# Optimization experiments

Measured on AMD Instinct MI355X. Metric: run time of the kernel, lower is better.

The kernel has to match this reference:

```python
import jax, jax.numpy as jnp
import numpy as np

N, K, D = 65536, 1024, 512


def setup_inputs() -> dict:
    key = jax.random.key(0)
    kx, kc, kv, kp = jax.random.split(key, 4)
    X = jax.random.normal(kx, (N, D), dtype=jnp.float32)
    center = jax.random.normal(kc, (K, D), dtype=jnp.float32)
    var = jax.random.uniform(kv, (K,), dtype=jnp.float32)
    pr = jax.random.uniform(kp, (K,), dtype=jnp.float32)
    threshold = jnp.zeros((1,), dtype=jnp.float32)
    return {"X": X, "center": center, "var": var, "pr": pr, "threshold": threshold}


def reference(X, center, var, pr, threshold):
    # Pairwise squared distances [N, K] via the expanded form
    # avoids materializing the N x K x D tensor).
    x_sq = jnp.sum(X * X, axis=-1, keepdims=True)            # [N, 1]
    c_sq = jnp.sum(center * center, axis=-1)                  # [K]
    cross = jnp.einsum('nd,kd->nk', X, center)                # [N, K]
    sqdist = x_sq - 2.0 * cross + c_sq[None, :]               # [N, K]
    # density: reciprocal-distance weighted sum with weights pr * var
    density = jnp.reciprocal(sqdist) @ (pr * var)             # [N]
    return density - threshold                                 # [N] (threshold [1] broadcasts)
```

## Files before the change

kernel.cpp:

```cpp
#include <hip/hip_runtime.h>
#include <stdint.h>


#define NR 65536
#define KC 1024
#define DD 512

#define BM 256
#define BN 256
#define BK 64
#define NKT (DD / BK)
#define NPART (KC / BN)

#define SLOT_SZ 65536
#define PART_OFF 131072
#define LDS_TOTAL (PART_OFF + 4096)

typedef __bf16 bf16;
typedef __attribute__((ext_vector_type(4))) __bf16 bf16x4;
typedef __attribute__((ext_vector_type(8))) __bf16 bf16x8;
typedef __attribute__((ext_vector_type(4))) float f32x4;

__device__ __forceinline__ void gload16(const void* g, void* l) {
  __builtin_amdgcn_global_load_lds(
      (const __attribute__((address_space(1))) unsigned int*)g,
      (__attribute__((address_space(3))) unsigned int*)l, 16, 0, 0);
}

__global__ __launch_bounds__(256) void prep_kernel(
    const float* __restrict__ X, const float* __restrict__ C,
    const float* __restrict__ var, const float* __restrict__ pr,
    bf16* __restrict__ Xb, bf16* __restrict__ Cb,
    float* __restrict__ xsq, float* __restrict__ csq, float* __restrict__ w) {
  const int row  = (int)((blockIdx.x * 256 + threadIdx.x) >> 6);
  const int lane = (int)(threadIdx.x & 63);
  const bool isX = row < NR;
  const float* srow = isX ? (X + (size_t)row * DD) : (C + (size_t)(row - NR) * DD);
  bf16* drow = isX ? (Xb + (size_t)row * DD) : (Cb + (size_t)(row - NR) * DD);

  float4 a = reinterpret_cast<const float4*>(srow)[lane];
  float4 b = reinterpret_cast<const float4*>(srow)[64 + lane];
  float s = a.x * a.x + a.y * a.y + a.z * a.z + a.w * a.w +
            b.x * b.x + b.y * b.y + b.z * b.z + b.w * b.w;
#pragma unroll
  for (int off = 1; off < 64; off <<= 1) s += __shfl_xor(s, off, 64);

  bf16x4 va = {(bf16)a.x, (bf16)a.y, (bf16)a.z, (bf16)a.w};
  bf16x4 vb = {(bf16)b.x, (bf16)b.y, (bf16)b.z, (bf16)b.w};
  reinterpret_cast<bf16x4*>(drow)[lane]      = va;
  reinterpret_cast<bf16x4*>(drow)[64 + lane] = vb;

  if (lane == 0) {
    if (isX) {
      xsq[row] = s;
    } else {
      const int k = row - NR;
      csq[k] = s;
      w[k]   = pr[k] * var[k];
    }
  }
}


#define STAGE_A(h, tn, slotW)                                                   \
  gload16(aSrc0 + (size_t)((h) * 64) * DD + (tn) * 64,                          \
          smem + (slotW) + (h) * 16384 + wid * 1024);                           \
  gload16(aSrc0 + (size_t)((h) * 64 + 128) * DD + (tn) * 64,                    \
          smem + (slotW) + (h) * 16384 + 8192 + wid * 1024);

#define STAGE_B(kk, tn, slotW)                                                  \
  gload16(bSrc0 + (tn) * 64 + (kk) * 32,                                        \
          smem + (slotW) + 32768 + (kk) * 16384 + wid * 1024);                  \
  gload16(bSrc0 + (size_t)128 * DD + (tn) * 64 + (kk) * 32,                     \
          smem + (slotW) + 32768 + (kk) * 16384 + 8192 + wid * 1024);

#define READ_B(dst, kk, base)                                                   \
  _Pragma("unroll") for (int n = 0; n < 4; ++n)                                 \
    dst[n] = *(const bf16x8*)(smem + (base) + 32768 + (kk) * 16384 + bRd +      \
                              n * 1024);

__global__ __launch_bounds__(512, 2) void density_kernel(
    const bf16* __restrict__ Xb, const bf16* __restrict__ Cb,
    const float* __restrict__ xsq, const float* __restrict__ csq,
    const float* __restrict__ w, float* __restrict__ partial) {
  extern __shared__ char smem[];

  const int tid  = (int)threadIdx.x;
  const int lane = tid & 63;
  const int wid  = tid >> 6;
  const int wr   = wid >> 2;
  const int wcn  = wid & 3;
  const int lr   = lane & 15;
  const int lc   = lane >> 4;

  const int bid   = (int)blockIdx.x;
  const int swz   = (bid & 7) * 128 + (bid >> 3);
  const int ntile = swz >> 8;
  const int mtile = swz & 255;
  const int rowBase = mtile * BM;
  const int colBase = ntile * BN;

  const bf16* aSrc0 = Xb + (size_t)(rowBase + wid * 8 + (lane >> 3)) * DD +
                      (((lane & 7) ^ (lane >> 3)) << 3);
  const bf16* bSrc0 = Cb + (size_t)(colBase + wid * 16 + (lane >> 2)) * DD +
                      ((((lane & 3) ^ ((lane >> 3) & 3))) << 3);

  const int aRd  = (wr * 64 + lr) * 128;
  const int aSw0 = ((lc ^ (lr & 7)) << 4);
  const int aSw1 = (((4 | lc) ^ (lr & 7)) << 4);
  const int bRd  = (wcn * 64 + lr) * 64 + ((lc ^ ((lr >> 1) & 3)) << 4);

  f32x4 acc[8][4];
#pragma unroll
  for (int m = 0; m < 8; ++m)
#pragma unroll
    for (int n = 0; n < 4; ++n) acc[m][n] = (f32x4){0.f, 0.f, 0.f, 0.f};

  bf16x8 bgK0[4], bgK1[4];

  STAGE_A(0, 0, 0);
  STAGE_B(0, 0, 0);
  STAGE_A(1, 0, 0);
  STAGE_B(1, 0, 0);
  asm volatile("s_waitcnt vmcnt(0)");
  __builtin_amdgcn_s_barrier();

#pragma unroll 1
  for (int t = 0; t < NKT; ++t) {
    const int slotR = (t & 1) << 16;
    const int slotW = slotR ^ SLOT_SZ;
    const int tn = t + 1;
    const bool st = tn < NKT;

    if (st) {
      STAGE_A(0, tn, slotW);
      STAGE_B(0, tn, slotW);
      STAGE_A(1, tn, slotW);
      STAGE_B(1, tn, slotW);
    }

    READ_B(bgK0, 0, slotR);
    READ_B(bgK1, 1, slotR);

    __builtin_amdgcn_s_setprio(1);
#pragma unroll
    for (int h = 0; h < 2; ++h) {
#pragma unroll
      for (int mi = 0; mi < 4; ++mi) {
        const bf16x8 a0 = *(const bf16x8*)(smem + slotR + h * 16384 + aRd +
                                           mi * 2048 + aSw0);
        const bf16x8 a1 = *(const bf16x8*)(smem + slotR + h * 16384 + aRd +
                                           mi * 2048 + aSw1);
#pragma unroll
        for (int n = 0; n < 4; ++n)
          acc[h * 4 + mi][n] = __builtin_amdgcn_mfma_f32_16x16x32_bf16(
              a0, bgK0[n], acc[h * 4 + mi][n], 0, 0, 0);
#pragma unroll
        for (int n = 0; n < 4; ++n)
          acc[h * 4 + mi][n] = __builtin_amdgcn_mfma_f32_16x16x32_bf16(
              a1, bgK1[n], acc[h * 4 + mi][n], 0, 0, 0);
      }
    }
    __builtin_amdgcn_s_setprio(0);

    if (st) {
      asm volatile("s_waitcnt vmcnt(0)");
      __builtin_amdgcn_s_barrier();
    }
  }

  float xr[8][4];
#pragma unroll
  for (int m = 0; m < 8; ++m)
#pragma unroll
    for (int j = 0; j < 4; ++j)
      xr[m][j] = xsq[rowBase + wr * 128 + m * 16 + lc * 4 + j];

  float rsum[8][4];
#pragma unroll
  for (int m = 0; m < 8; ++m)
#pragma unroll
    for (int j = 0; j < 4; ++j) rsum[m][j] = 0.f;

#pragma unroll
  for (int n = 0; n < 4; ++n) {
    const int gc = colBase + wcn * 64 + n * 16 + lr;
    const float cs = csq[gc];
    const float ww = w[gc];
#pragma unroll
    for (int m = 0; m < 8; ++m)
#pragma unroll
      for (int j = 0; j < 4; ++j) {
        const float sq = xr[m][j] + cs - 2.f * acc[m][n][j];
        rsum[m][j] += ww * __builtin_amdgcn_rcpf(sq);
      }
  }
#pragma unroll
  for (int m = 0; m < 8; ++m)
#pragma unroll
    for (int j = 0; j < 4; ++j) {
      float v = rsum[m][j];
      v += __shfl_xor(v, 1, 64);
      v += __shfl_xor(v, 2, 64);
      v += __shfl_xor(v, 4, 64);
      v += __shfl_xor(v, 8, 64);
      rsum[m][j] = v;
    }

  float* part = (float*)(smem + PART_OFF);
  __syncthreads();
  if (lr == 0) {
#pragma unroll
    for (int m = 0; m < 8; ++m)
#pragma unroll
      for (int j = 0; j < 4; ++j)
        part[wcn * 256 + wr * 128 + m * 16 + lc * 4 + j] = rsum[m][j];
  }
  __syncthreads();
  if (tid < BM) {
    const float s = part[tid] + part[256 + tid] + part[512 + tid] + part[768 + tid];
    partial[(size_t)ntile * NR + rowBase + tid] = s;
  }
}

__global__ __launch_bounds__(256) void reduce_kernel(
    const float* __restrict__ partial, const float* __restrict__ thr,
    float* __restrict__ out) {
  const int n = (int)(blockIdx.x * 256 + threadIdx.x);
  float s = 0.f;
#pragma unroll
  for (int g = 0; g < NPART; ++g) s += partial[(size_t)g * NR + n];
  out[n] = s - thr[0];
}

extern "C" void kernel_launch(void* const* d_in, const int* in_sizes, int n_in,
                              void* d_out, int out_size, void* d_ws, size_t ws_size,
                              hipStream_t stream) {
  const float* X   = (const float*)d_in[0];
  const float* C   = (const float*)d_in[1];
  const float* var = (const float*)d_in[2];
  const float* pr  = (const float*)d_in[3];
  const float* thr = (const float*)d_in[4];
  float* out = (float*)d_out;

  char* ws = (char*)d_ws;
  bf16* Xb   = (bf16*)(ws);
  bf16* Cb   = (bf16*)(ws + (size_t)NR * DD * 2);
  float* xsq = (float*)(ws + (size_t)NR * DD * 2 + (size_t)KC * DD * 2);
  float* csq = xsq + NR;
  float* w   = csq + KC;
  float* partial = w + KC;

  prep_kernel<<<(NR + KC) / 4, 256, 0, stream>>>(X, C, var, pr, Xb, Cb, xsq, csq, w);
  density_kernel<<<(NR / BM) * NPART, 512, LDS_TOTAL, stream>>>(
      Xb, Cb, xsq, csq, w, partial);
  reduce_kernel<<<NR / 256, 256, 0, stream>>>(partial, thr, out);
}
```

Before: 114.8 us.

## Shrink density GEMM tile to 128x256 with BK=32 and four waves

Reworks the density GEMM tiling from 256x256 blocks of 8 waves with BK=64 to 128x256 blocks of 4 waves with BK=32. LDS use drops from about 132KB to about 50KB, and the grid doubles to 2048 blocks, so more blocks can be resident per CU and waves are spread more evenly across CUs. The cost is lower arithmetic intensity per block, more X/C reloads from L2, and twice as many k-iterations, each with its own barrier.

```diff
diff --git a/kernel.cpp b/kernel.cpp
--- a/kernel.cpp
+++ b/kernel.cpp
@@ -6,15 +6,15 @@
 #define KC 1024
 #define DD 512
 
-#define BM 256
+#define BM 128
 #define BN 256
-#define BK 64
+#define BK 32
 #define NKT (DD / BK)
 #define NPART (KC / BN)
 
-#define SLOT_SZ 65536
-#define PART_OFF 131072
-#define LDS_TOTAL (PART_OFF + 4096)
+#define SLOT_SZ 24576
+#define PART_OFF 49152
+#define LDS_TOTAL (PART_OFF + 2048)
 
 typedef __bf16 bf16;
 typedef __attribute__((ext_vector_type(4))) __bf16 bf16x4;
@@ -62,24 +62,19 @@
 }
 
 
-#define STAGE_A(h, tn, slotW)                                                   \
-  gload16(aSrc0 + (size_t)((h) * 64) * DD + (tn) * 64,                          \
-          smem + (slotW) + (h) * 16384 + wid * 1024);                           \
-  gload16(aSrc0 + (size_t)((h) * 64 + 128) * DD + (tn) * 64,                    \
-          smem + (slotW) + (h) * 16384 + 8192 + wid * 1024);
-
-#define STAGE_B(kk, tn, slotW)                                                  \
-  gload16(bSrc0 + (tn) * 64 + (kk) * 32,                                        \
-          smem + (slotW) + 32768 + (kk) * 16384 + wid * 1024);                  \
-  gload16(bSrc0 + (size_t)128 * DD + (tn) * 64 + (kk) * 32,                     \
-          smem + (slotW) + 32768 + (kk) * 16384 + 8192 + wid * 1024);
-
-#define READ_B(dst, kk, base)                                                   \
-  _Pragma("unroll") for (int n = 0; n < 4; ++n)                                 \
-    dst[n] = *(const bf16x8*)(smem + (base) + 32768 + (kk) * 16384 + bRd +      \
-                              n * 1024);
-
-__global__ __launch_bounds__(512, 2) void density_kernel(
+#define STAGE(tn, slotW)                                                        \
+  gload16(aSrc0 + (tn) * 32,                smem + (slotW) + wid * 1024);       \
+  gload16(aSrc0 + (size_t)64 * DD + (tn) * 32,                                  \
+          smem + (slotW) + 4096 + wid * 1024);                                  \
+  gload16(bSrc0 + (tn) * 32,                smem + (slotW) + 8192 + wid * 1024);\
+  gload16(bSrc0 + (size_t)64 * DD + (tn) * 32,                                  \
+          smem + (slotW) + 12288 + wid * 1024);                                 \
+  gload16(bSrc0 + (size_t)128 * DD + (tn) * 32,                                 \
+          smem + (slotW) + 16384 + wid * 1024);                                 \
+  gload16(bSrc0 + (size_t)192 * DD + (tn) * 32,                                 \
+          smem + (slotW) + 20480 + wid * 1024);
+
+__global__ __launch_bounds__(256, 2) void density_kernel(
     const bf16* __restrict__ Xb, const bf16* __restrict__ Cb,
     const float* __restrict__ xsq, const float* __restrict__ csq,
     const float* __restrict__ w, float* __restrict__ partial) {
@@ -88,27 +83,23 @@
   const int tid  = (int)threadIdx.x;
   const int lane = tid & 63;
   const int wid  = tid >> 6;
-  const int wr   = wid >> 2;
-  const int wcn  = wid & 3;
   const int lr   = lane & 15;
   const int lc   = lane >> 4;
 
   const int bid   = (int)blockIdx.x;
-  const int swz   = (bid & 7) * 128 + (bid >> 3);
-  const int ntile = swz >> 8;
-  const int mtile = swz & 255;
+  const int swz   = (bid & 7) * 256 + (bid >> 3);
+  const int ntile = swz >> 9;
+  const int mtile = swz & 511;
   const int rowBase = mtile * BM;
   const int colBase = ntile * BN;
 
-  const bf16* aSrc0 = Xb + (size_t)(rowBase + wid * 8 + (lane >> 3)) * DD +
-                      (((lane & 7) ^ (lane >> 3)) << 3);
-  const bf16* bSrc0 = Cb + (size_t)(colBase + wid * 16 + (lane >> 2)) * DD +
-                      ((((lane & 3) ^ ((lane >> 3) & 3))) << 3);
-
-  const int aRd  = (wr * 64 + lr) * 128;
-  const int aSw0 = ((lc ^ (lr & 7)) << 4);
-  const int aSw1 = (((4 | lc) ^ (lr & 7)) << 4);
-  const int bRd  = (wcn * 64 + lr) * 64 + ((lc ^ ((lr >> 1) & 3)) << 4);
+  const int chunkSw = (((lane & 3) ^ ((lane >> 3) & 3)) << 3);
+  const bf16* aSrc0 = Xb + (size_t)(rowBase + wid * 16 + (lane >> 2)) * DD + chunkSw;
+  const bf16* bSrc0 = Cb + (size_t)(colBase + wid * 16 + (lane >> 2)) * DD + chunkSw;
+
+  const int rdSw = ((lc ^ ((lr >> 1) & 3)) << 4);
+  const int aRd  = lr * 64 + rdSw;
+  const int bRd  = 8192 + (wid * 64 + lr) * 64 + rdSw;
 
   f32x4 acc[8][4];
 #pragma unroll
@@ -116,50 +107,34 @@
 #pragma unroll
     for (int n = 0; n < 4; ++n) acc[m][n] = (f32x4){0.f, 0.f, 0.f, 0.f};
 
-  bf16x8 bgK0[4], bgK1[4];
-
-  STAGE_A(0, 0, 0);
-  STAGE_B(0, 0, 0);
-  STAGE_A(1, 0, 0);
-  STAGE_B(1, 0, 0);
+  STAGE(0, 0);
   asm volatile("s_waitcnt vmcnt(0)");
   __builtin_amdgcn_s_barrier();
 
 #pragma unroll 1
   for (int t = 0; t < NKT; ++t) {
-    const int slotR = (t & 1) << 16;
+    const int slotR = (t & 1) ? SLOT_SZ : 0;
     const int slotW = slotR ^ SLOT_SZ;
     const int tn = t + 1;
     const bool st = tn < NKT;
 
     if (st) {
-      STAGE_A(0, tn, slotW);
-      STAGE_B(0, tn, slotW);
-      STAGE_A(1, tn, slotW);
-      STAGE_B(1, tn, slotW);
-    }
-
-    READ_B(bgK0, 0, slotR);
-    READ_B(bgK1, 1, slotR);
+      STAGE(tn, slotW);
+    }
+
+    bf16x8 bg[4];
+#pragma unroll
+    for (int n = 0; n < 4; ++n)
+      bg[n] = *(const bf16x8*)(smem + slotR + bRd + n * 1024);
 
     __builtin_amdgcn_s_setprio(1);
 #pragma unroll
-    for (int h = 0; h < 2; ++h) {
-#pragma unroll
-      for (int mi = 0; mi < 4; ++mi) {
-        const bf16x8 a0 = *(const bf16x8*)(smem + slotR + h * 16384 + aRd +
-                                           mi * 2048 + aSw0);
-        const bf16x8 a1 = *(const bf16x8*)(smem + slotR + h * 16384 + aRd +
-                                           mi * 2048 + aSw1);
-#pragma unroll
-        for (int n = 0; n < 4; ++n)
-          acc[h * 4 + mi][n] = __builtin_amdgcn_mfma_f32_16x16x32_bf16(
-              a0, bgK0[n], acc[h * 4 + mi][n], 0, 0, 0);
-#pragma unroll
-        for (int n = 0; n < 4; ++n)
-          acc[h * 4 + mi][n] = __builtin_amdgcn_mfma_f32_16x16x32_bf16(
-              a1, bgK1[n], acc[h * 4 + mi][n], 0, 0, 0);
-      }
+    for (int mi = 0; mi < 8; ++mi) {
+      const bf16x8 a = *(const bf16x8*)(smem + slotR + aRd + mi * 1024);
+#pragma unroll
+      for (int n = 0; n < 4; ++n)
+        acc[mi][n] = __builtin_amdgcn_mfma_f32_16x16x32_bf16(
+            a, bg[n], acc[mi][n], 0, 0, 0);
     }
     __builtin_amdgcn_s_setprio(0);
 
@@ -174,7 +149,7 @@
   for (int m = 0; m < 8; ++m)
 #pragma unroll
     for (int j = 0; j < 4; ++j)
-      xr[m][j] = xsq[rowBase + wr * 128 + m * 16 + lc * 4 + j];
+      xr[m][j] = xsq[rowBase + m * 16 + lc * 4 + j];
 
   float rsum[8][4];
 #pragma unroll
@@ -184,7 +159,7 @@
 
 #pragma unroll
   for (int n = 0; n < 4; ++n) {
-    const int gc = colBase + wcn * 64 + n * 16 + lr;
+    const int gc = colBase + wid * 64 + n * 16 + lr;
     const float cs = csq[gc];
     const float ww = w[gc];
 #pragma unroll
@@ -214,11 +189,11 @@
     for (int m = 0; m < 8; ++m)
 #pragma unroll
       for (int j = 0; j < 4; ++j)
-        part[wcn * 256 + wr * 128 + m * 16 + lc * 4 + j] = rsum[m][j];
+        part[wid * 128 + m * 16 + lc * 4 + j] = rsum[m][j];
   }
   __syncthreads();
   if (tid < BM) {
-    const float s = part[tid] + part[256 + tid] + part[512 + tid] + part[768 + tid];
+    const float s = part[tid] + part[128 + tid] + part[256 + tid] + part[384 + tid];
     partial[(size_t)ntile * NR + rowBase + tid] = s;
   }
 }
@@ -252,7 +227,7 @@
   float* partial = w + KC;
 
   prep_kernel<<<(NR + KC) / 4, 256, 0, stream>>>(X, C, var, pr, Xb, Cb, xsq, csq, w);
-  density_kernel<<<(NR / BM) * NPART, 512, LDS_TOTAL, stream>>>(
+  density_kernel<<<(NR / BM) * NPART, 256, LDS_TOTAL, stream>>>(
       Xb, Cb, xsq, csq, w, partial);
   reduce_kernel<<<NR / 256, 256, 0, stream>>>(partial, thr, out);
 }
```

Result: slower. 120.0 us (+4.5%).

## Split K-tile compute into four phases interleaving LDS reads, prefetch and MFMA

Applied to the files above, without the earlier changes.

Restructures the main loop into four phases per K tile. Each phase reads one quarter of the A fragments (and B fragments as needed), issues one quarter of the next tile's global-to-LDS prefetch, then runs its MFMAs after barriers. This follows the ping-pong style of interleaving memory and math across the two resident waves per SIMD, so loads spread out instead of bursting. The trade is many more barriers per tile, which adds synchronisation overhead and may stall waves.

```diff
diff --git a/kernel.cpp b/kernel.cpp
--- a/kernel.cpp
+++ b/kernel.cpp
@@ -116,8 +116,6 @@
 #pragma unroll
     for (int n = 0; n < 4; ++n) acc[m][n] = (f32x4){0.f, 0.f, 0.f, 0.f};
 
-  bf16x8 bgK0[4], bgK1[4];
-
   STAGE_A(0, 0, 0);
   STAGE_B(0, 0, 0);
   STAGE_A(1, 0, 0);
@@ -132,40 +130,49 @@
     const int tn = t + 1;
     const bool st = tn < NKT;
 
-    if (st) {
-      STAGE_A(0, tn, slotW);
-      STAGE_B(0, tn, slotW);
-      STAGE_A(1, tn, slotW);
-      STAGE_B(1, tn, slotW);
-    }
-
-    READ_B(bgK0, 0, slotR);
-    READ_B(bgK1, 1, slotR);
-
-    __builtin_amdgcn_s_setprio(1);
-#pragma unroll
-    for (int h = 0; h < 2; ++h) {
+    bf16x8 bgK0[4], bgK1[4];
+
+#pragma unroll
+    for (int p = 0; p < 4; ++p) {
+      const int h  = p >> 1;
+      const int kk = p & 1;
+
+      if (p == 0) { READ_B(bgK0, 0, slotR); }
+      if (p == 1) { READ_B(bgK1, 1, slotR); }
+
+      bf16x8 af[4];
+#pragma unroll
+      for (int mi = 0; mi < 4; ++mi)
+        af[mi] = *(const bf16x8*)(smem + slotR + h * 16384 + aRd + mi * 2048 +
+                                  (kk ? aSw1 : aSw0));
+
+      if (st) {
+        if (p == 0) { STAGE_A(0, tn, slotW); }
+        if (p == 1) { STAGE_A(1, tn, slotW); }
+        if (p == 2) { STAGE_B(0, tn, slotW); }
+        if (p == 3) { STAGE_B(1, tn, slotW); }
+      }
+
+      __builtin_amdgcn_s_barrier();
+      asm volatile("s_waitcnt lgkmcnt(0)" ::: "memory");
+
+      __builtin_amdgcn_s_setprio(1);
 #pragma unroll
       for (int mi = 0; mi < 4; ++mi) {
-        const bf16x8 a0 = *(const bf16x8*)(smem + slotR + h * 16384 + aRd +
-                                           mi * 2048 + aSw0);
-        const bf16x8 a1 = *(const bf16x8*)(smem + slotR + h * 16384 + aRd +
-                                           mi * 2048 + aSw1);
-#pragma unroll
-        for (int n = 0; n < 4; ++n)
-          acc[h * 4 + mi][n] = __builtin_amdgcn_mfma_f32_16x16x32_bf16(
-              a0, bgK0[n], acc[h * 4 + mi][n], 0, 0, 0);
-#pragma unroll
-        for (int n = 0; n < 4; ++n)
-          acc[h * 4 + mi][n] = __builtin_amdgcn_mfma_f32_16x16x32_bf16(
-              a1, bgK1[n], acc[h * 4 + mi][n], 0, 0, 0);
+#pragma unroll
+        for (int n = 0; n < 4; ++n) {
+          if (kk == 0)
+            acc[h * 4 + mi][n] = __builtin_amdgcn_mfma_f32_16x16x32_bf16(
+                af[mi], bgK0[n], acc[h * 4 + mi][n], 0, 0, 0);
+          else
+            acc[h * 4 + mi][n] = __builtin_amdgcn_mfma_f32_16x16x32_bf16(
+                af[mi], bgK1[n], acc[h * 4 + mi][n], 0, 0, 0);
+        }
       }
-    }
-    __builtin_amdgcn_s_setprio(0);
-
-    if (st) {
-      asm volatile("s_waitcnt vmcnt(0)");
-      __builtin_amdgcn_s_barrier();
+      __builtin_amdgcn_s_setprio(0);
+
+      if (p == 3 && st) asm volatile("s_waitcnt vmcnt(0)" ::: "memory");
+      if (p < 3 || st) __builtin_amdgcn_s_barrier();
     }
   }
 
```

After: 117.6 us. 2.5% more time.

## Fuse X bf16 conversion and panel reduction into a single density kernel

Applied to the files above, without the earlier changes.

Drops the separate X-to-bf16 prep pass and the partial-sum reduce kernel. Each block now walks all four center panels itself. It loads fp32 X straight into registers, converts it to bf16 while writing the swizzled LDS tile, and computes the row norms on the fly during the first panel. The threshold-subtracted result is written directly to the output. This removes the Xb workspace round trip and one launch. In exchange, fp32 X is re-read once per panel, the grid shrinks to one block per row tile with lower occupancy, and A staging now goes through registers instead of direct global-to-LDS loads.

```diff
diff --git a/kernel.cpp b/kernel.cpp
--- a/kernel.cpp
+++ b/kernel.cpp
@@ -10,11 +10,12 @@
 #define BN 256
 #define BK 64
 #define NKT (DD / BK)
-#define NPART (KC / BN)
+#define NPANEL (KC / BN)
 
 #define SLOT_SZ 65536
 #define PART_OFF 131072
-#define LDS_TOTAL (PART_OFF + 4096)
+#define XSQ_OFF  135168
+#define LDS_TOTAL (XSQ_OFF + 1024)
 
 typedef __bf16 bf16;
 typedef __attribute__((ext_vector_type(4))) __bf16 bf16x4;
@@ -27,16 +28,14 @@
       (__attribute__((address_space(3))) unsigned int*)l, 16, 0, 0);
 }
 
-__global__ __launch_bounds__(256) void prep_kernel(
-    const float* __restrict__ X, const float* __restrict__ C,
-    const float* __restrict__ var, const float* __restrict__ pr,
-    bf16* __restrict__ Xb, bf16* __restrict__ Cb,
-    float* __restrict__ xsq, float* __restrict__ csq, float* __restrict__ w) {
+__global__ __launch_bounds__(256) void prep_c(
+    const float* __restrict__ C, const float* __restrict__ var,
+    const float* __restrict__ pr, bf16* __restrict__ Cb,
+    float* __restrict__ csq, float* __restrict__ w) {
   const int row  = (int)((blockIdx.x * 256 + threadIdx.x) >> 6);
   const int lane = (int)(threadIdx.x & 63);
-  const bool isX = row < NR;
-  const float* srow = isX ? (X + (size_t)row * DD) : (C + (size_t)(row - NR) * DD);
-  bf16* drow = isX ? (Xb + (size_t)row * DD) : (Cb + (size_t)(row - NR) * DD);
+  const float* srow = C + (size_t)row * DD;
+  bf16* drow = Cb + (size_t)row * DD;
 
   float4 a = reinterpret_cast<const float4*>(srow)[lane];
   float4 b = reinterpret_cast<const float4*>(srow)[64 + lane];
@@ -51,22 +50,36 @@
   reinterpret_cast<bf16x4*>(drow)[64 + lane] = vb;
 
   if (lane == 0) {
-    if (isX) {
-      xsq[row] = s;
-    } else {
-      const int k = row - NR;
-      csq[k] = s;
-      w[k]   = pr[k] * var[k];
-    }
-  }
-}
-
-
-#define STAGE_A(h, tn, slotW)                                                   \
-  gload16(aSrc0 + (size_t)((h) * 64) * DD + (tn) * 64,                          \
-          smem + (slotW) + (h) * 16384 + wid * 1024);                           \
-  gload16(aSrc0 + (size_t)((h) * 64 + 128) * DD + (tn) * 64,                    \
-          smem + (slotW) + (h) * 16384 + 8192 + wid * 1024);
+    csq[row] = s;
+    w[row]   = pr[row] * var[row];
+  }
+}
+
+
+#define AOFF(g) ((g) == 0 ? 0 : (g) == 1 ? 128 * DD : (g) == 2 ? 64 * DD : 192 * DD)
+
+#define A_LOAD(dst, tn)                                                         \
+  _Pragma("unroll") for (int g = 0; g < 4; ++g) {                               \
+    const float* s_ = aSrcF + AOFF(g) + (tn) * 64;                              \
+    dst[2 * g]     = *(const f32x4*)(s_);                                       \
+    dst[2 * g + 1] = *(const f32x4*)(s_ + 4);                                   \
+  }
+
+#define A_WRITE(src, slotW)                                                     \
+  _Pragma("unroll") for (int g = 0; g < 4; ++g) {                               \
+    bf16x8 v_;                                                                  \
+    _Pragma("unroll") for (int e = 0; e < 4; ++e) {                             \
+      v_[e]     = (bf16)src[2 * g][e];                                          \
+      v_[4 + e] = (bf16)src[2 * g + 1][e];                                      \
+    }                                                                           \
+    *(bf16x8*)(smem + (slotW) + g * 8192 + wid * 1024 + lane * 16) = v_;        \
+  }
+
+#define XSQACC(src)                                                             \
+  _Pragma("unroll") for (int g = 0; g < 4; ++g)                                 \
+    _Pragma("unroll") for (int e = 0; e < 4; ++e)                               \
+      xa[g] += src[2 * g][e] * src[2 * g][e] +                                  \
+               src[2 * g + 1][e] * src[2 * g + 1][e];
 
 #define STAGE_B(kk, tn, slotW)                                                  \
   gload16(bSrc0 + (tn) * 64 + (kk) * 32,                                        \
@@ -79,10 +92,10 @@
     dst[n] = *(const bf16x8*)(smem + (base) + 32768 + (kk) * 16384 + bRd +      \
                               n * 1024);
 
-__global__ __launch_bounds__(512, 2) void density_kernel(
-    const bf16* __restrict__ Xb, const bf16* __restrict__ Cb,
-    const float* __restrict__ xsq, const float* __restrict__ csq,
-    const float* __restrict__ w, float* __restrict__ partial) {
+__global__ __launch_bounds__(512) void density_kernel(
+    const float* __restrict__ X, const bf16* __restrict__ Cb,
+    const float* __restrict__ csq, const float* __restrict__ w,
+    const float* __restrict__ thr, float* __restrict__ out) {
   extern __shared__ char smem[];
 
   const int tid  = (int)threadIdx.x;
@@ -93,108 +106,132 @@
   const int lr   = lane & 15;
   const int lc   = lane >> 4;
 
-  const int bid   = (int)blockIdx.x;
-  const int swz   = (bid & 7) * 128 + (bid >> 3);
-  const int ntile = swz >> 8;
-  const int mtile = swz & 255;
-  const int rowBase = mtile * BM;
-  const int colBase = ntile * BN;
-
-  const bf16* aSrc0 = Xb + (size_t)(rowBase + wid * 8 + (lane >> 3)) * DD +
-                      (((lane & 7) ^ (lane >> 3)) << 3);
-  const bf16* bSrc0 = Cb + (size_t)(colBase + wid * 16 + (lane >> 2)) * DD +
-                      ((((lane & 3) ^ ((lane >> 3) & 3))) << 3);
+  const int rowBase = (int)blockIdx.x * BM;
+  const float th = thr[0];
+
+  const int rowL   = wid * 8 + (lane >> 3);
+  const int dchunk = ((lane & 7) ^ (lane >> 3)) << 3;
+  const float* aSrcF = X + (size_t)(rowBase + rowL) * DD + dchunk;
+
+  const int chunkSwB = (((lane & 3) ^ ((lane >> 3) & 3)) << 3);
 
   const int aRd  = (wr * 64 + lr) * 128;
   const int aSw0 = ((lc ^ (lr & 7)) << 4);
   const int aSw1 = (((4 | lc) ^ (lr & 7)) << 4);
   const int bRd  = (wcn * 64 + lr) * 64 + ((lc ^ ((lr >> 1) & 3)) << 4);
 
-  f32x4 acc[8][4];
+  float rsum[8][4];
 #pragma unroll
   for (int m = 0; m < 8; ++m)
 #pragma unroll
-    for (int n = 0; n < 4; ++n) acc[m][n] = (f32x4){0.f, 0.f, 0.f, 0.f};
-
-  bf16x8 bgK0[4], bgK1[4];
-
-  STAGE_A(0, 0, 0);
-  STAGE_B(0, 0, 0);
-  STAGE_A(1, 0, 0);
-  STAGE_B(1, 0, 0);
-  asm volatile("s_waitcnt vmcnt(0)");
-  __builtin_amdgcn_s_barrier();
+    for (int j = 0; j < 4; ++j) rsum[m][j] = 0.f;
+
+  float xa[4] = {0.f, 0.f, 0.f, 0.f};
+  f32x4 xrv[8];
+  f32x4 areg[8];
 
 #pragma unroll 1
-  for (int t = 0; t < NKT; ++t) {
-    const int slotR = (t & 1) << 16;
-    const int slotW = slotR ^ SLOT_SZ;
-    const int tn = t + 1;
-    const bool st = tn < NKT;
-
-    if (st) {
-      STAGE_A(0, tn, slotW);
-      STAGE_B(0, tn, slotW);
-      STAGE_A(1, tn, slotW);
-      STAGE_B(1, tn, slotW);
-    }
-
-    READ_B(bgK0, 0, slotR);
-    READ_B(bgK1, 1, slotR);
-
-    __builtin_amdgcn_s_setprio(1);
-#pragma unroll
-    for (int h = 0; h < 2; ++h) {
-#pragma unroll
-      for (int mi = 0; mi < 4; ++mi) {
-        const bf16x8 a0 = *(const bf16x8*)(smem + slotR + h * 16384 + aRd +
-                                           mi * 2048 + aSw0);
-        const bf16x8 a1 = *(const bf16x8*)(smem + slotR + h * 16384 + aRd +
-                                           mi * 2048 + aSw1);
-#pragma unroll
-        for (int n = 0; n < 4; ++n)
-          acc[h * 4 + mi][n] = __builtin_amdgcn_mfma_f32_16x16x32_bf16(
-              a0, bgK0[n], acc[h * 4 + mi][n], 0, 0, 0);
-#pragma unroll
-        for (int n = 0; n < 4; ++n)
-          acc[h * 4 + mi][n] = __builtin_amdgcn_mfma_f32_16x16x32_bf16(
-              a1, bgK1[n], acc[h * 4 + mi][n], 0, 0, 0);
-      }
-    }
-    __builtin_amdgcn_s_setprio(0);
-
-    if (st) {
-      asm volatile("s_waitcnt vmcnt(0)");
-      __builtin_amdgcn_s_barrier();
-    }
-  }
-
-  float xr[8][4];
-#pragma unroll
-  for (int m = 0; m < 8; ++m)
-#pragma unroll
-    for (int j = 0; j < 4; ++j)
-      xr[m][j] = xsq[rowBase + wr * 128 + m * 16 + lc * 4 + j];
-
-  float rsum[8][4];
-#pragma unroll
-  for (int m = 0; m < 8; ++m)
-#pragma unroll
-    for (int j = 0; j < 4; ++j) rsum[m][j] = 0.f;
-
-#pragma unroll
-  for (int n = 0; n < 4; ++n) {
-    const int gc = colBase + wcn * 64 + n * 16 + lr;
-    const float cs = csq[gc];
-    const float ww = w[gc];
+  for (int p = 0; p < NPANEL; ++p) {
+    const int colBase = p * BN;
+    const bf16* bSrc0 = Cb + (size_t)(colBase + wid * 16 + (lane >> 2)) * DD +
+                        chunkSwB;
+
+    f32x4 acc[8][4];
 #pragma unroll
     for (int m = 0; m < 8; ++m)
 #pragma unroll
-      for (int j = 0; j < 4; ++j) {
-        const float sq = xr[m][j] + cs - 2.f * acc[m][n][j];
-        rsum[m][j] += ww * __builtin_amdgcn_rcpf(sq);
-      }
-  }
+      for (int n = 0; n < 4; ++n) acc[m][n] = (f32x4){0.f, 0.f, 0.f, 0.f};
+
+    A_LOAD(areg, 0);
+    STAGE_B(0, 0, 0);
+    STAGE_B(1, 0, 0);
+    asm volatile("s_waitcnt vmcnt(0)" ::: "memory");
+    A_WRITE(areg, 0);
+    if (p == 0) { XSQACC(areg); }
+    asm volatile("s_waitcnt lgkmcnt(0)" ::: "memory");
+    __builtin_amdgcn_s_barrier();
+
+#pragma unroll 1
+    for (int t = 0; t < NKT; ++t) {
+      const int slotR = (t & 1) << 16;
+      const int slotW = slotR ^ SLOT_SZ;
+      const bool st = (t + 1) < NKT;
+
+      if (st) {
+        A_LOAD(areg, t + 1);
+        STAGE_B(0, t + 1, slotW);
+        STAGE_B(1, t + 1, slotW);
+      }
+
+      bf16x8 bgK0[4], bgK1[4];
+      READ_B(bgK0, 0, slotR);
+      READ_B(bgK1, 1, slotR);
+
+      __builtin_amdgcn_s_setprio(1);
+#pragma unroll
+      for (int h = 0; h < 2; ++h) {
+#pragma unroll
+        for (int mi = 0; mi < 4; ++mi) {
+          const bf16x8 a0 = *(const bf16x8*)(smem + slotR + h * 16384 + aRd +
+                                             mi * 2048 + aSw0);
+          const bf16x8 a1 = *(const bf16x8*)(smem + slotR + h * 16384 + aRd +
+                                             mi * 2048 + aSw1);
+#pragma unroll
+          for (int n = 0; n < 4; ++n)
+            acc[h * 4 + mi][n] = __builtin_amdgcn_mfma_f32_16x16x32_bf16(
+                a0, bgK0[n], acc[h * 4 + mi][n], 0, 0, 0);
+#pragma unroll
+          for (int n = 0; n < 4; ++n)
+            acc[h * 4 + mi][n] = __builtin_amdgcn_mfma_f32_16x16x32_bf16(
+                a1, bgK1[n], acc[h * 4 + mi][n], 0, 0, 0);
+        }
+      }
+      __builtin_amdgcn_s_setprio(0);
+
+      if (st) {
+        asm volatile("s_waitcnt vmcnt(0)" ::: "memory");
+        A_WRITE(areg, slotW);
+        if (p == 0) { XSQACC(areg); }
+        asm volatile("s_waitcnt lgkmcnt(0)" ::: "memory");
+        __builtin_amdgcn_s_barrier();
+      }
+    }
+
+    if (p == 0) {
+#pragma unroll
+      for (int off = 1; off < 8; off <<= 1) {
+#pragma unroll
+        for (int g = 0; g < 4; ++g) xa[g] += __shfl_xor(xa[g], off, 64);
+      }
+      float* xsqS = (float*)(smem + XSQ_OFF);
+      if ((lane & 7) == 0) {
+        const int r0 = wid * 8 + (lane >> 3);
+        xsqS[r0]       = xa[0];
+        xsqS[r0 + 128] = xa[1];
+        xsqS[r0 + 64]  = xa[2];
+        xsqS[r0 + 192] = xa[3];
+      }
+      __syncthreads();
+#pragma unroll
+      for (int m = 0; m < 8; ++m)
+        xrv[m] = *(const f32x4*)(xsqS + wr * 128 + m * 16 + lc * 4);
+    }
+
+#pragma unroll
+    for (int n = 0; n < 4; ++n) {
+      const int gc = colBase + wcn * 64 + n * 16 + lr;
+      const float cs = csq[gc];
+      const float ww = w[gc];
+#pragma unroll
+      for (int m = 0; m < 8; ++m)
+#pragma unroll
+        for (int j = 0; j < 4; ++j) {
+          const float sq = xrv[m][j] + cs - 2.f * acc[m][n][j];
+          rsum[m][j] += ww * __builtin_amdgcn_rcpf(sq);
+        }
+    }
+  }
+
 #pragma unroll
   for (int m = 0; m < 8; ++m)
 #pragma unroll
@@ -219,18 +256,8 @@
   __syncthreads();
   if (tid < BM) {
     const float s = part[tid] + part[256 + tid] + part[512 + tid] + part[768 + tid];
-    partial[(size_t)ntile * NR + rowBase + tid] = s;
-  }
-}
-
-__global__ __launch_bounds__(256) void reduce_kernel(
-    const float* __restrict__ partial, const float* __restrict__ thr,
-    float* __restrict__ out) {
-  const int n = (int)(blockIdx.x * 256 + threadIdx.x);
-  float s = 0.f;
-#pragma unroll
-  for (int g = 0; g < NPART; ++g) s += partial[(size_t)g * NR + n];
-  out[n] = s - thr[0];
+    out[rowBase + tid] = s - th;
+  }
 }
 
 extern "C" void kernel_launch(void* const* d_in, const int* in_sizes, int n_in,
@@ -244,15 +271,10 @@
   float* out = (float*)d_out;
 
   char* ws = (char*)d_ws;
-  bf16* Xb   = (bf16*)(ws);
-  bf16* Cb   = (bf16*)(ws + (size_t)NR * DD * 2);
-  float* xsq = (float*)(ws + (size_t)NR * DD * 2 + (size_t)KC * DD * 2);
-  float* csq = xsq + NR;
+  bf16* Cb   = (bf16*)(ws);
+  float* csq = (float*)(ws + (size_t)KC * DD * 2);
   float* w   = csq + KC;
-  float* partial = w + KC;
-
-  prep_kernel<<<(NR + KC) / 4, 256, 0, stream>>>(X, C, var, pr, Xb, Cb, xsq, csq, w);
-  density_kernel<<<(NR / BM) * NPART, 512, LDS_TOTAL, stream>>>(
-      Xb, Cb, xsq, csq, w, partial);
-  reduce_kernel<<<NR / 256, 256, 0, stream>>>(partial, thr, out);
-}
+
+  prep_c<<<KC / 4, 256, 0, stream>>>(C, var, pr, Cb, csq, w);
+  density_kernel<<<NR / BM, 512, LDS_TOTAL, stream>>>(X, Cb, csq, w, thr, out);
+}
```

Measured after the change: 145.5 us. 1.27x slower.
